# Performance work log

Hardware: AMD Instinct MI355X
Metric: run time of the kernel (lower is better)

## Reference

```python
import jax, jax.numpy as jnp
import numpy as np

B, E, D, O = 2048, 64, 512, 512  # batch, n_options, latent_dim, out_dim


def setup_inputs() -> dict:
    key = jax.random.key(0)
    k1, k2, k3, k4 = jax.random.split(key, 4)
    bound = 1.0 / np.sqrt(D)  # kaiming/fan_in-style scale
    x = jax.random.normal(k1, (B, D), dtype=jnp.float32)
    option = jax.random.randint(k2, (B,), 0, E, dtype=jnp.int32)
    weight = jax.random.uniform(k3, (E, D, O), dtype=jnp.float32, minval=-bound, maxval=bound)
    bias = jax.random.uniform(k4, (E, O), dtype=jnp.float32, minval=-bound, maxval=bound)
    return {"x": x, "option": option, "weight": weight, "bias": bias}


def reference(x, option, weight, bias):
    # out[b] = x[b] @ weight[option[b]] + bias[option[b]]
    w_g = jnp.take(weight, option, axis=0)          # [B, D, O] per-sample gathered weights
    b_g = jnp.take(bias, option, axis=0)            # [B, O]
    out = jnp.einsum('bd,bdo->bo', x, w_g) + b_g    # [B, O]
    return out
```

## Files before the change

kernel.cpp:

```cpp
#include <hip/hip_runtime.h>

#define B_N 2048
#define E_N 64
#define D_N 512
#define O_N 512
#define ON  64
#define MC  32
#define XS_LD 520

typedef __bf16 bf16x8 __attribute__((ext_vector_type(8)));
typedef float  f32x4  __attribute__((ext_vector_type(4)));

__device__ __forceinline__ unsigned short f2bf(float f) {
  unsigned int u = __float_as_uint(f);
  u = (u + 0x7FFFu + ((u >> 16) & 1u)) >> 16;
  return (unsigned short)u;
}

__global__ void bucket_kernel(const int* __restrict__ opt,
                              int* __restrict__ cnt,
                              int* __restrict__ list) {
  __shared__ int scnt[E_N];
  const int t = threadIdx.x;
  if (t < E_N) scnt[t] = 0;
  __syncthreads();
#pragma unroll
  for (int i = 0; i < B_N / 1024; ++i) {
    int b = t + i * 1024;
    int e = opt[b];
    int slot = atomicAdd(&scnt[e], 1);
    list[e * B_N + slot] = b;
  }
  __syncthreads();
  if (t < E_N) cnt[t] = scnt[t];
}

__global__ __launch_bounds__(256)
void gemm_kernel(const float* __restrict__ x,
                 const float* __restrict__ w,
                 const float* __restrict__ bias,
                 const int* __restrict__ cnt,
                 const int* __restrict__ list,
                 float* __restrict__ out) {
  __shared__ unsigned short xs[MC * XS_LD];

  const int e    = blockIdx.x;
  const int o0   = blockIdx.y * ON;
  const int t    = threadIdx.x;
  const int lane = t & 63;
  const int wave = t >> 6;
  const int n    = cnt[e];
  const float* wexp = w + (size_t)e * D_N * O_N;
  const int m_in = lane & 15;
  const int g    = lane >> 4;
  const int col  = o0 + wave * 16 + m_in;
  const float bval = bias[e * O_N + col];
  const int* mylist = list + e * B_N;

  for (int m0 = 0; m0 < n; m0 += MC) {
    __syncthreads();
#pragma unroll
    for (int i = 0; i < 16; ++i) {
      int idx = t + i * 256;
      int row = idx >> 7;
      int c4  = idx & 127;
      int s   = m0 + row;
      unsigned short v0 = 0, v1 = 0, v2 = 0, v3 = 0;
      if (s < n) {
        int b = mylist[s];
        const float4 xv = *reinterpret_cast<const float4*>(x + (size_t)b * D_N + c4 * 4);
        v0 = f2bf(xv.x); v1 = f2bf(xv.y); v2 = f2bf(xv.z); v3 = f2bf(xv.w);
      }
      *reinterpret_cast<ushort4*>(&xs[row * XS_LD + c4 * 4]) = make_ushort4(v0, v1, v2, v3);
    }
    __syncthreads();

    f32x4 acc0 = {0.f, 0.f, 0.f, 0.f};
    f32x4 acc1 = {0.f, 0.f, 0.f, 0.f};

    for (int k0 = 0; k0 < D_N; k0 += 32) {
      const int kb = k0 + g * 8;
      union { uint4 u; bf16x8 v; } a0, a1;
      a0.u = *reinterpret_cast<const uint4*>(&xs[m_in * XS_LD + kb]);
      a1.u = *reinterpret_cast<const uint4*>(&xs[(m_in + 16) * XS_LD + kb]);
      union { unsigned short u[8]; bf16x8 v; } bf;
      const float* wp = wexp + (size_t)kb * O_N + col;
#pragma unroll
      for (int j = 0; j < 8; ++j) bf.u[j] = f2bf(wp[(size_t)j * O_N]);

      acc0 = __builtin_amdgcn_mfma_f32_16x16x32_bf16(a0.v, bf.v, acc0, 0, 0, 0);
      acc1 = __builtin_amdgcn_mfma_f32_16x16x32_bf16(a1.v, bf.v, acc1, 0, 0, 0);
    }

#pragma unroll
    for (int r = 0; r < 4; ++r) {
      int sl = g * 4 + r;
      int s  = m0 + sl;
      if (s < n)      out[(size_t)mylist[s]  * O_N + col] = acc0[r] + bval;
      int s2 = m0 + 16 + sl;
      if (s2 < n)     out[(size_t)mylist[s2] * O_N + col] = acc1[r] + bval;
    }
  }
}

extern "C" void kernel_launch(void* const* d_in, const int* in_sizes, int n_in,
                              void* d_out, int out_size, void* d_ws, size_t ws_size,
                              hipStream_t stream) {
  const float* x      = (const float*)d_in[0];
  const int*   option = (const int*)d_in[1];
  const float* weight = (const float*)d_in[2];
  const float* bias   = (const float*)d_in[3];
  float* out = (float*)d_out;

  int* cnt  = (int*)d_ws;
  int* list = (int*)((char*)d_ws + 256);

  bucket_kernel<<<1, 1024, 0, stream>>>(option, cnt, list);
  gemm_kernel<<<dim3(E_N, O_N / ON), 256, 0, stream>>>(x, weight, bias, cnt, list, out);
}
```

Measured before the change: 33.39 us.

## Double the row chunk to 64 with 512 threads and software-pipeline weight loads

Each block now runs 8 waves over 64 rows: two wave groups share the same weight columns and handle different 32-row halves. Expert weights are prefetched into registers one k-step ahead (double-buffered bu/bn) so global load latency overlaps the MFMAs. Blocks for experts with zero rows exit early. With about 32 rows per expert, half the waves will often do padded work, and register pressure rises.

```diff
diff --git a/kernel.cpp b/kernel.cpp
--- a/kernel.cpp
+++ b/kernel.cpp
@@ -5,7 +5,7 @@
 #define D_N 512
 #define O_N 512
 #define ON  64
-#define MC  32
+#define MC  64
 #define XS_LD 520
 
 typedef __bf16 bf16x8 __attribute__((ext_vector_type(8)));
@@ -13,6 +13,10 @@
 
 __device__ __forceinline__ unsigned short f2bf(float f) {
   unsigned int u = __float_as_uint(f);
+  u = (u + 0x7FFFu + ((u >> 16) & 1u)) >> 16;
+  return (unsigned short)u;
+}
+__device__ __forceinline__ unsigned short u2bf(unsigned int u) {
   u = (u + 0x7FFFu + ((u >> 16) & 1u)) >> 16;
   return (unsigned short)u;
 }
@@ -35,7 +39,7 @@
   if (t < E_N) cnt[t] = scnt[t];
 }
 
-__global__ __launch_bounds__(256)
+__global__ __launch_bounds__(512)
 void gemm_kernel(const float* __restrict__ x,
                  const float* __restrict__ w,
                  const float* __restrict__ bias,
@@ -49,55 +53,87 @@
   const int t    = threadIdx.x;
   const int lane = t & 63;
   const int wave = t >> 6;
+  const int wc   = wave & 3;
+  const int wg   = wave >> 2;
   const int n    = cnt[e];
+  if (n == 0) return;
+
   const float* wexp = w + (size_t)e * D_N * O_N;
   const int m_in = lane & 15;
   const int g    = lane >> 4;
-  const int col  = o0 + wave * 16 + m_in;
+  const int col  = o0 + wc * 16 + m_in;
   const float bval = bias[e * O_N + col];
   const int* mylist = list + e * B_N;
+  const int arow0 = (wg * 32 + m_in) * XS_LD;
 
   for (int m0 = 0; m0 < n; m0 += MC) {
     __syncthreads();
 #pragma unroll
     for (int i = 0; i < 16; ++i) {
-      int idx = t + i * 256;
+      int idx = t + i * 512;
       int row = idx >> 7;
       int c4  = idx & 127;
       int s   = m0 + row;
-      unsigned short v0 = 0, v1 = 0, v2 = 0, v3 = 0;
+      ushort4 v = make_ushort4(0, 0, 0, 0);
       if (s < n) {
-        int b = mylist[s];
-        const float4 xv = *reinterpret_cast<const float4*>(x + (size_t)b * D_N + c4 * 4);
-        v0 = f2bf(xv.x); v1 = f2bf(xv.y); v2 = f2bf(xv.z); v3 = f2bf(xv.w);
+        const float4 xv = *reinterpret_cast<const float4*>(x + (size_t)mylist[s] * D_N + c4 * 4);
+        v = make_ushort4(f2bf(xv.x), f2bf(xv.y), f2bf(xv.z), f2bf(xv.w));
       }
-      *reinterpret_cast<ushort4*>(&xs[row * XS_LD + c4 * 4]) = make_ushort4(v0, v1, v2, v3);
+      *reinterpret_cast<ushort4*>(&xs[row * XS_LD + c4 * 4]) = v;
     }
     __syncthreads();
 
     f32x4 acc0 = {0.f, 0.f, 0.f, 0.f};
     f32x4 acc1 = {0.f, 0.f, 0.f, 0.f};
 
-    for (int k0 = 0; k0 < D_N; k0 += 32) {
-      const int kb = k0 + g * 8;
-      union { uint4 u; bf16x8 v; } a0, a1;
-      a0.u = *reinterpret_cast<const uint4*>(&xs[m_in * XS_LD + kb]);
-      a1.u = *reinterpret_cast<const uint4*>(&xs[(m_in + 16) * XS_LD + kb]);
-      union { unsigned short u[8]; bf16x8 v; } bf;
-      const float* wp = wexp + (size_t)kb * O_N + col;
+    unsigned bu[8], bn[8];
+    {
+      const float* wp = wexp + (size_t)(g * 8) * O_N + col;
 #pragma unroll
-      for (int j = 0; j < 8; ++j) bf.u[j] = f2bf(wp[(size_t)j * O_N]);
+      for (int j = 0; j < 8; ++j) bu[j] = __float_as_uint(wp[(size_t)j * O_N]);
+    }
 
-      acc0 = __builtin_amdgcn_mfma_f32_16x16x32_bf16(a0.v, bf.v, acc0, 0, 0, 0);
-      acc1 = __builtin_amdgcn_mfma_f32_16x16x32_bf16(a1.v, bf.v, acc1, 0, 0, 0);
+    for (int k0 = 0; k0 < D_N; k0 += 64) {
+      {
+        const float* wp = wexp + (size_t)(k0 + 32 + g * 8) * O_N + col;
+#pragma unroll
+        for (int j = 0; j < 8; ++j) bn[j] = __float_as_uint(wp[(size_t)j * O_N]);
+      }
+      {
+        const int kb = arow0 + k0 + g * 8;
+        union { uint4 u; bf16x8 v; } a0, a1;
+        a0.u = *reinterpret_cast<const uint4*>(&xs[kb]);
+        a1.u = *reinterpret_cast<const uint4*>(&xs[kb + 16 * XS_LD]);
+        union { unsigned short us[8]; bf16x8 v; } bf;
+#pragma unroll
+        for (int j = 0; j < 8; ++j) bf.us[j] = u2bf(bu[j]);
+        acc0 = __builtin_amdgcn_mfma_f32_16x16x32_bf16(a0.v, bf.v, acc0, 0, 0, 0);
+        acc1 = __builtin_amdgcn_mfma_f32_16x16x32_bf16(a1.v, bf.v, acc1, 0, 0, 0);
+      }
+      {
+        const float* wp = wexp + (size_t)(((k0 + 64) & (D_N - 1)) + g * 8) * O_N + col;
+#pragma unroll
+        for (int j = 0; j < 8; ++j) bu[j] = __float_as_uint(wp[(size_t)j * O_N]);
+      }
+      {
+        const int kb = arow0 + k0 + 32 + g * 8;
+        union { uint4 u; bf16x8 v; } a0, a1;
+        a0.u = *reinterpret_cast<const uint4*>(&xs[kb]);
+        a1.u = *reinterpret_cast<const uint4*>(&xs[kb + 16 * XS_LD]);
+        union { unsigned short us[8]; bf16x8 v; } bf;
+#pragma unroll
+        for (int j = 0; j < 8; ++j) bf.us[j] = u2bf(bn[j]);
+        acc0 = __builtin_amdgcn_mfma_f32_16x16x32_bf16(a0.v, bf.v, acc0, 0, 0, 0);
+        acc1 = __builtin_amdgcn_mfma_f32_16x16x32_bf16(a1.v, bf.v, acc1, 0, 0, 0);
+      }
     }
 
 #pragma unroll
     for (int r = 0; r < 4; ++r) {
-      int sl = g * 4 + r;
+      int sl = wg * 32 + g * 4 + r;
       int s  = m0 + sl;
       if (s < n)      out[(size_t)mylist[s]  * O_N + col] = acc0[r] + bval;
-      int s2 = m0 + 16 + sl;
+      int s2 = m0 + sl + 16;
       if (s2 < n)     out[(size_t)mylist[s2] * O_N + col] = acc1[r] + bval;
     }
   }
@@ -116,5 +152,5 @@
   int* list = (int*)((char*)d_ws + 256);
 
   bucket_kernel<<<1, 1024, 0, stream>>>(option, cnt, list);
-  gemm_kernel<<<dim3(E_N, O_N / ON), 256, 0, stream>>>(x, weight, bias, cnt, list, out);
+  gemm_kernel<<<dim3(E_N, O_N / ON), 512, 0, stream>>>(x, weight, bias, cnt, list, out);
 }
```

Measured after the change: 34.44 us. 1.03x slower.

## Stage expert weights through double-buffered LDS via async DMA, widen row tile

Applied to the files above, without the earlier changes.

Expert weight tiles are now streamed into LDS with global_load_lds into two ping-pong buffers, so the next k-slice loads while the current one is computed. Before, the kernel did strided per-thread global loads inside the MFMA loop. The block grows to 512 threads covering 64 rows, which halves weight reloads per expert. The x tile uses an XOR swizzle in place of padding. Bucketing now uses a multi-block kernel with global atomics plus a memset, which adds one more launch and makes the list order nondeterministic.

```diff
diff --git a/kernel.cpp b/kernel.cpp
--- a/kernel.cpp
+++ b/kernel.cpp
@@ -5,8 +5,8 @@
 #define D_N 512
 #define O_N 512
 #define ON  64
-#define MC  32
-#define XS_LD 520
+#define MC  64
+#define NT  16
 
 typedef __bf16 bf16x8 __attribute__((ext_vector_type(8)));
 typedef float  f32x4  __attribute__((ext_vector_type(4)));
@@ -17,88 +17,113 @@
   return (unsigned short)u;
 }
 
-__global__ void bucket_kernel(const int* __restrict__ opt,
-                              int* __restrict__ cnt,
-                              int* __restrict__ list) {
-  __shared__ int scnt[E_N];
-  const int t = threadIdx.x;
-  if (t < E_N) scnt[t] = 0;
-  __syncthreads();
-#pragma unroll
-  for (int i = 0; i < B_N / 1024; ++i) {
-    int b = t + i * 1024;
-    int e = opt[b];
-    int slot = atomicAdd(&scnt[e], 1);
-    list[e * B_N + slot] = b;
-  }
-  __syncthreads();
-  if (t < E_N) cnt[t] = scnt[t];
+__global__ __launch_bounds__(256)
+void bucket_kernel(const int* __restrict__ opt, int* __restrict__ cnt,
+                   int* __restrict__ list) {
+  int b = blockIdx.x * 256 + threadIdx.x;
+  int e = opt[b];
+  int slot = atomicAdd(&cnt[e], 1);
+  list[e * B_N + slot] = b;
 }
 
-__global__ __launch_bounds__(256)
-void gemm_kernel(const float* __restrict__ x,
-                 const float* __restrict__ w,
-                 const float* __restrict__ bias,
-                 const int* __restrict__ cnt,
-                 const int* __restrict__ list,
-                 float* __restrict__ out) {
-  __shared__ unsigned short xs[MC * XS_LD];
+__device__ __forceinline__ void step_compute(
+    const unsigned short* __restrict__ xs, const float* __restrict__ wsp,
+    int kt, int g, int col64, int r0, int r1, f32x4& acc0, f32x4& acc1) {
+  const int kb = kt * 32 + g * 8;
+  const int key = (r0 & 7) << 3;
+  union { uint4 u; bf16x8 v; } a0, a1;
+  a0.u = *reinterpret_cast<const uint4*>(&xs[r0 * 512 + ((kb ^ key))]);
+  a1.u = *reinterpret_cast<const uint4*>(&xs[r1 * 512 + ((kb ^ key))]);
+  union { unsigned short us[8]; bf16x8 v; } bf_;
+  const int csw = col64 ^ (g << 4);
+#pragma unroll
+  for (int j = 0; j < 8; ++j) bf_.us[j] = f2bf(wsp[(g * 8 + j) * 64 + csw]);
+  acc0 = __builtin_amdgcn_mfma_f32_16x16x32_bf16(a0.v, bf_.v, acc0, 0, 0, 0);
+  acc1 = __builtin_amdgcn_mfma_f32_16x16x32_bf16(a1.v, bf_.v, acc1, 0, 0, 0);
+}
+
+#define DMA_W(KT, WSBUF) do {                                                  \
+    const float* _src = wexp + (size_t)((KT) * 32 + dk) * O_N + o0 + scol;     \
+    __builtin_amdgcn_global_load_lds(                                          \
+        (const __attribute__((address_space(1))) void*)_src,                   \
+        (__attribute__((address_space(3))) void*)&WSBUF[wave * 256], 16, 0, 0);\
+  } while (0)
+
+#define WAIT1_BAR() asm volatile("s_waitcnt vmcnt(1)\ns_barrier" ::: "memory")
+#define WAIT0_BAR() asm volatile("s_waitcnt vmcnt(0)\ns_barrier" ::: "memory")
+#define LGKM_BAR()  asm volatile("s_waitcnt lgkmcnt(0)\ns_barrier" ::: "memory")
+
+__global__ __launch_bounds__(512)
+void gemm_kernel(const float* __restrict__ x, const float* __restrict__ w,
+                 const float* __restrict__ bias, const int* __restrict__ cnt,
+                 const int* __restrict__ list, float* __restrict__ out) {
+  __shared__ unsigned short xs[MC * 512];
+  __shared__ float wsA[32 * 64];
+  __shared__ float wsB[32 * 64];
 
   const int e    = blockIdx.x;
   const int o0   = blockIdx.y * ON;
   const int t    = threadIdx.x;
   const int lane = t & 63;
   const int wave = t >> 6;
+  const int wc   = wave & 3;
+  const int wg   = wave >> 2;
   const int n    = cnt[e];
+  if (n == 0) return;
+
   const float* wexp = w + (size_t)e * D_N * O_N;
-  const int m_in = lane & 15;
-  const int g    = lane >> 4;
-  const int col  = o0 + wave * 16 + m_in;
-  const float bval = bias[e * O_N + col];
+  const int m_in  = lane & 15;
+  const int g     = lane >> 4;
+  const int col64 = wc * 16 + m_in;
+  const float bval = bias[e * O_N + o0 + col64];
   const int* mylist = list + e * B_N;
+  const int r0 = wg * 32 + m_in;
+  const int r1 = r0 + 16;
+
+  const int dk   = 4 * wave + (lane >> 4);
+  const int skey = ((dk >> 3) & 3) << 4;
+  const int scol = ((lane & 15) * 4) ^ skey;
 
   for (int m0 = 0; m0 < n; m0 += MC) {
     __syncthreads();
+    DMA_W(0, wsA);
 #pragma unroll
     for (int i = 0; i < 16; ++i) {
-      int idx = t + i * 256;
+      int idx = t + i * 512;
       int row = idx >> 7;
       int c4  = idx & 127;
       int s   = m0 + row;
-      unsigned short v0 = 0, v1 = 0, v2 = 0, v3 = 0;
+      ushort4 v = make_ushort4(0, 0, 0, 0);
       if (s < n) {
-        int b = mylist[s];
-        const float4 xv = *reinterpret_cast<const float4*>(x + (size_t)b * D_N + c4 * 4);
-        v0 = f2bf(xv.x); v1 = f2bf(xv.y); v2 = f2bf(xv.z); v3 = f2bf(xv.w);
+        const float4 xv = *reinterpret_cast<const float4*>(x + (size_t)mylist[s] * D_N + c4 * 4);
+        v = make_ushort4(f2bf(xv.x), f2bf(xv.y), f2bf(xv.z), f2bf(xv.w));
       }
-      *reinterpret_cast<ushort4*>(&xs[row * XS_LD + c4 * 4]) = make_ushort4(v0, v1, v2, v3);
+      *reinterpret_cast<ushort4*>(&xs[row * 512 + ((c4 * 4) ^ ((row & 7) << 3))]) = v;
     }
     __syncthreads();
 
     f32x4 acc0 = {0.f, 0.f, 0.f, 0.f};
     f32x4 acc1 = {0.f, 0.f, 0.f, 0.f};
 
-    for (int k0 = 0; k0 < D_N; k0 += 32) {
-      const int kb = k0 + g * 8;
-      union { uint4 u; bf16x8 v; } a0, a1;
-      a0.u = *reinterpret_cast<const uint4*>(&xs[m_in * XS_LD + kb]);
-      a1.u = *reinterpret_cast<const uint4*>(&xs[(m_in + 16) * XS_LD + kb]);
-      union { unsigned short u[8]; bf16x8 v; } bf;
-      const float* wp = wexp + (size_t)kb * O_N + col;
-#pragma unroll
-      for (int j = 0; j < 8; ++j) bf.u[j] = f2bf(wp[(size_t)j * O_N]);
-
-      acc0 = __builtin_amdgcn_mfma_f32_16x16x32_bf16(a0.v, bf.v, acc0, 0, 0, 0);
-      acc1 = __builtin_amdgcn_mfma_f32_16x16x32_bf16(a1.v, bf.v, acc1, 0, 0, 0);
+#pragma unroll 1
+    for (int kt = 0; kt < NT; kt += 2) {
+      DMA_W(kt + 1, wsB);
+      WAIT1_BAR();
+      step_compute(xs, wsA, kt, g, col64, r0, r1, acc0, acc1);
+      LGKM_BAR();
+      if (kt + 2 < NT) { DMA_W(kt + 2, wsA); WAIT1_BAR(); }
+      else             { WAIT0_BAR(); }
+      step_compute(xs, wsB, kt + 1, g, col64, r0, r1, acc0, acc1);
+      LGKM_BAR();
     }
 
 #pragma unroll
     for (int r = 0; r < 4; ++r) {
-      int sl = g * 4 + r;
+      int sl = wg * 32 + g * 4 + r;
       int s  = m0 + sl;
-      if (s < n)      out[(size_t)mylist[s]  * O_N + col] = acc0[r] + bval;
-      int s2 = m0 + 16 + sl;
-      if (s2 < n)     out[(size_t)mylist[s2] * O_N + col] = acc1[r] + bval;
+      if (s < n)  out[(size_t)mylist[s]  * O_N + o0 + col64] = acc0[r] + bval;
+      int s2 = m0 + sl + 16;
+      if (s2 < n) out[(size_t)mylist[s2] * O_N + o0 + col64] = acc1[r] + bval;
     }
   }
 }
@@ -115,6 +140,7 @@
   int* cnt  = (int*)d_ws;
   int* list = (int*)((char*)d_ws + 256);
 
-  bucket_kernel<<<1, 1024, 0, stream>>>(option, cnt, list);
-  gemm_kernel<<<dim3(E_N, O_N / ON), 256, 0, stream>>>(x, weight, bias, cnt, list, out);
+  hipMemsetAsync(cnt, 0, E_N * sizeof(int), stream);
+  bucket_kernel<<<B_N / 256, 256, 0, stream>>>(option, cnt, list);
+  gemm_kernel<<<dim3(E_N, O_N / ON), 512, 0, stream>>>(x, weight, bias, cnt, list, out);
 }
```

New measurement: 33.18 us. Within noise of the previous version (-0.6%).

## Split-K grouped GEMM with LDS-cached bf16 weight slice and atomic accumulation

Applied to the files above, without the earlier changes.

Each block now owns one expert and a 64-wide K slice. It converts that weight slice to bf16 once into swizzled LDS and then holds the B fragments in registers across all token chunks, instead of re-reading and re-converting fp32 weights per token chunk. The bias is pre-written into the output by a separate kernel, and partial sums are combined with float atomicAdd into the output. The bucketing kernel becomes multi-block with global atomics after a memset. The trade-offs are more kernel launches, heavy float atomic traffic, and nondeterministic summation order.

```diff
diff --git a/kernel.cpp b/kernel.cpp
--- a/kernel.cpp
+++ b/kernel.cpp
@@ -1,105 +1,146 @@
 #include <hip/hip_runtime.h>
+#include <hip/hip_bf16.h>
 
 #define B_N 2048
 #define E_N 64
 #define D_N 512
 #define O_N 512
-#define ON  64
-#define MC  32
-#define XS_LD 520
+#define NSL 8
+#define KS  64
+#define XLD 72
 
 typedef __bf16 bf16x8 __attribute__((ext_vector_type(8)));
 typedef float  f32x4  __attribute__((ext_vector_type(4)));
 
-__device__ __forceinline__ unsigned short f2bf(float f) {
-  unsigned int u = __float_as_uint(f);
-  u = (u + 0x7FFFu + ((u >> 16) & 1u)) >> 16;
-  return (unsigned short)u;
-}
-
-__global__ void bucket_kernel(const int* __restrict__ opt,
-                              int* __restrict__ cnt,
-                              int* __restrict__ list) {
-  __shared__ int scnt[E_N];
-  const int t = threadIdx.x;
-  if (t < E_N) scnt[t] = 0;
-  __syncthreads();
-#pragma unroll
-  for (int i = 0; i < B_N / 1024; ++i) {
-    int b = t + i * 1024;
-    int e = opt[b];
-    int slot = atomicAdd(&scnt[e], 1);
-    list[e * B_N + slot] = b;
-  }
-  __syncthreads();
-  if (t < E_N) cnt[t] = scnt[t];
+__device__ __forceinline__ unsigned cvt2(float a, float b) {
+  union { __hip_bfloat162 h; unsigned u; } c;
+  c.h = __float22bfloat162_rn(make_float2(a, b));
+  return c.u;
 }
 
 __global__ __launch_bounds__(256)
-void gemm_kernel(const float* __restrict__ x,
-                 const float* __restrict__ w,
-                 const float* __restrict__ bias,
-                 const int* __restrict__ cnt,
-                 const int* __restrict__ list,
+void bucket_kernel(const int* __restrict__ opt, int* __restrict__ cnt,
+                   int* __restrict__ list) {
+  int b = blockIdx.x * 256 + threadIdx.x;
+  int e = opt[b];
+  int slot = atomicAdd(&cnt[e], 1);
+  list[e * B_N + slot] = b;
+}
+
+__global__ __launch_bounds__(256)
+void bias_init_kernel(const int* __restrict__ opt, const float* __restrict__ bias,
+                      float* __restrict__ out) {
+  int gid = blockIdx.x * 256 + threadIdx.x;
+  int b  = gid >> 7;
+  int o4 = gid & 127;
+  int e  = opt[b];
+  reinterpret_cast<float4*>(out)[(size_t)b * 128 + o4] =
+      reinterpret_cast<const float4*>(bias)[(size_t)e * 128 + o4];
+}
+
+__global__ __launch_bounds__(512, 4)
+void gemm_kernel(const float* __restrict__ x, const float* __restrict__ w,
+                 const int* __restrict__ cnt, const int* __restrict__ list,
                  float* __restrict__ out) {
-  __shared__ unsigned short xs[MC * XS_LD];
+  __shared__ unsigned short ws[KS * 512];
+  __shared__ unsigned short xs[64 * XLD];
+  __shared__ int sl[64];
 
   const int e    = blockIdx.x;
-  const int o0   = blockIdx.y * ON;
+  const int s    = blockIdx.y;
   const int t    = threadIdx.x;
   const int lane = t & 63;
   const int wave = t >> 6;
   const int n    = cnt[e];
-  const float* wexp = w + (size_t)e * D_N * O_N;
+  if (n == 0) return;
+
   const int m_in = lane & 15;
   const int g    = lane >> 4;
-  const int col  = o0 + wave * 16 + m_in;
-  const float bval = bias[e * O_N + col];
   const int* mylist = list + e * B_N;
 
-  for (int m0 = 0; m0 < n; m0 += MC) {
-    __syncthreads();
+  const float* wsl = w + (size_t)e * D_N * O_N + (size_t)s * KS * O_N;
 #pragma unroll
-    for (int i = 0; i < 16; ++i) {
-      int idx = t + i * 256;
-      int row = idx >> 7;
-      int c4  = idx & 127;
-      int s   = m0 + row;
-      unsigned short v0 = 0, v1 = 0, v2 = 0, v3 = 0;
-      if (s < n) {
-        int b = mylist[s];
-        const float4 xv = *reinterpret_cast<const float4*>(x + (size_t)b * D_N + c4 * 4);
-        v0 = f2bf(xv.x); v1 = f2bf(xv.y); v2 = f2bf(xv.z); v3 = f2bf(xv.w);
+  for (int i = 0; i < 16; ++i) {
+    int idx = t + i * 512;
+    int k   = idx >> 7;
+    int c0  = (idx & 127) * 4;
+    const float4 f = *reinterpret_cast<const float4*>(wsl + (size_t)idx * 4);
+    *reinterpret_cast<uint2*>(&ws[k * 512 + (c0 ^ ((k & 15) << 2))]) =
+        make_uint2(cvt2(f.x, f.y), cvt2(f.z, f.w));
+  }
+  __syncthreads();
+
+  union { unsigned short us[8]; bf16x8 v; } frag[4][2];
+#pragma unroll
+  for (int cg = 0; cg < 4; ++cg) {
+    const int c = wave * 64 + cg * 16 + m_in;
+#pragma unroll
+    for (int ks = 0; ks < 2; ++ks) {
+#pragma unroll
+      for (int j = 0; j < 8; ++j) {
+        const int kk = ks * 32 + g * 8 + j;
+        frag[cg][ks].us[j] = ws[kk * 512 + (c ^ ((kk & 15) << 2))];
       }
-      *reinterpret_cast<ushort4*>(&xs[row * XS_LD + c4 * 4]) = make_ushort4(v0, v1, v2, v3);
+    }
+  }
+
+  for (int m0 = 0; m0 < n; m0 += 64) {
+#pragma unroll
+    for (int i = 0; i < 2; ++i) {
+      int idx = t + i * 512;
+      int row = idx >> 4;
+      int c4  = idx & 15;
+      int sm  = m0 + row;
+      uint2 v = make_uint2(0u, 0u);
+      int b = 0;
+      if (sm < n) {
+        b = mylist[sm];
+        const float4 xv = *reinterpret_cast<const float4*>(
+            x + (size_t)b * D_N + s * KS + c4 * 4);
+        v = make_uint2(cvt2(xv.x, xv.y), cvt2(xv.z, xv.w));
+      }
+      if (c4 == 0) sl[row] = b;
+      *reinterpret_cast<uint2*>(&xs[row * XLD + c4 * 4]) = v;
     }
     __syncthreads();
 
-    f32x4 acc0 = {0.f, 0.f, 0.f, 0.f};
-    f32x4 acc1 = {0.f, 0.f, 0.f, 0.f};
-
-    for (int k0 = 0; k0 < D_N; k0 += 32) {
-      const int kb = k0 + g * 8;
-      union { uint4 u; bf16x8 v; } a0, a1;
-      a0.u = *reinterpret_cast<const uint4*>(&xs[m_in * XS_LD + kb]);
-      a1.u = *reinterpret_cast<const uint4*>(&xs[(m_in + 16) * XS_LD + kb]);
-      union { unsigned short u[8]; bf16x8 v; } bf;
-      const float* wp = wexp + (size_t)kb * O_N + col;
 #pragma unroll
-      for (int j = 0; j < 8; ++j) bf.u[j] = f2bf(wp[(size_t)j * O_N]);
-
-      acc0 = __builtin_amdgcn_mfma_f32_16x16x32_bf16(a0.v, bf.v, acc0, 0, 0, 0);
-      acc1 = __builtin_amdgcn_mfma_f32_16x16x32_bf16(a1.v, bf.v, acc1, 0, 0, 0);
-    }
+    for (int mc = 0; mc < 2; ++mc) {
+      f32x4 acc[2][4];
+#pragma unroll
+      for (int rg = 0; rg < 2; ++rg)
+#pragma unroll
+        for (int cg = 0; cg < 4; ++cg) acc[rg][cg] = (f32x4){0.f, 0.f, 0.f, 0.f};
 
 #pragma unroll
-    for (int r = 0; r < 4; ++r) {
-      int sl = g * 4 + r;
-      int s  = m0 + sl;
-      if (s < n)      out[(size_t)mylist[s]  * O_N + col] = acc0[r] + bval;
-      int s2 = m0 + 16 + sl;
-      if (s2 < n)     out[(size_t)mylist[s2] * O_N + col] = acc1[r] + bval;
+      for (int ks = 0; ks < 2; ++ks) {
+        union { uint4 u; bf16x8 v; } a0, a1;
+        a0.u = *reinterpret_cast<const uint4*>(
+            &xs[(mc * 32 + m_in) * XLD + ks * 32 + g * 8]);
+        a1.u = *reinterpret_cast<const uint4*>(
+            &xs[(mc * 32 + 16 + m_in) * XLD + ks * 32 + g * 8]);
+#pragma unroll
+        for (int cg = 0; cg < 4; ++cg) {
+          acc[0][cg] = __builtin_amdgcn_mfma_f32_16x16x32_bf16(
+              a0.v, frag[cg][ks].v, acc[0][cg], 0, 0, 0);
+          acc[1][cg] = __builtin_amdgcn_mfma_f32_16x16x32_bf16(
+              a1.v, frag[cg][ks].v, acc[1][cg], 0, 0, 0);
+        }
+      }
+
+#pragma unroll
+      for (int rg = 0; rg < 2; ++rg)
+#pragma unroll
+        for (int cg = 0; cg < 4; ++cg)
+#pragma unroll
+          for (int r = 0; r < 4; ++r) {
+            int rl = mc * 32 + rg * 16 + g * 4 + r;
+            if (m0 + rl < n)
+              atomicAdd(&out[(size_t)sl[rl] * O_N + wave * 64 + cg * 16 + m_in],
+                        acc[rg][cg][r]);
+          }
     }
+    __syncthreads();
   }
 }
 
@@ -115,6 +156,8 @@
   int* cnt  = (int*)d_ws;
   int* list = (int*)((char*)d_ws + 256);
 
-  bucket_kernel<<<1, 1024, 0, stream>>>(option, cnt, list);
-  gemm_kernel<<<dim3(E_N, O_N / ON), 256, 0, stream>>>(x, weight, bias, cnt, list, out);
+  hipMemsetAsync(cnt, 0, E_N * sizeof(int), stream);
+  bucket_kernel<<<B_N / 256, 256, 0, stream>>>(option, cnt, list);
+  bias_init_kernel<<<(B_N * O_N / 4) / 256, 256, 0, stream>>>(option, bias, out);
+  gemm_kernel<<<dim3(E_N, NSL), 512, 0, stream>>>(x, weight, cnt, list, out);
 }
```

Result: slower. 53.98 us (+61.7%).
